# Optimization experiments

Hardware: AMD Instinct MI355X
Metric: run time of the kernel (lower is better)

The kernel has to match this reference:

```python
import jax, jax.numpy as jnp
import numpy as np

N, D, P, R, T, K = 200000, 128, 4096, 4, 3, 16

def setup_inputs() -> dict:
    key = jax.random.key(0)
    ks = jax.random.split(key, 9)
    return {
        "node_embeds": jax.random.normal(ks[0], (N, D), jnp.float32),
        "node_pairs": jax.random.randint(ks[1], (P, 2), 0, N),
        "node_type_ids": jax.random.randint(ks[2], (N,), 0, T),
        "neighbor_idx": jax.random.randint(ks[3], (P, 2, R, K), 0, N),
        "delta_t": jax.random.uniform(ks[4], (P, 2, R, K), jnp.float32),
        "W_phi": jax.random.normal(ks[5], (T, D, D), jnp.float32) * 0.05,
        "W_zeta": jax.random.normal(ks[6], (2 * D,), jnp.float32) * 0.05,
        "W_beta_w": jax.random.normal(ks[7], (R, D, D), jnp.float32) * 0.05,
        "W_beta_b": jax.random.normal(ks[8], (R, D), jnp.float32) * 0.05,
    }

def reference(node_embeds, node_pairs, node_type_ids, neighbor_idx, delta_t,
              W_phi, W_zeta, W_beta_w, W_beta_b):
    n = node_embeds.shape[0]
    # per-node type-specific linear: compute all types then select (T small)
    H_all = jnp.einsum('nd,tde->tne', node_embeds, W_phi)        # [T,N,D]
    H = H_all[node_type_ids, jnp.arange(n)]                      # [N,D]
    # micro attention: e = W_zeta([h_n; h_s]) * exp(-dt), softmax over K neighbors
    zn, zs = W_zeta[:D], W_zeta[D:]
    h_n = H[neighbor_idx]                                        # [P,2,R,K,D]
    e_n = jnp.einsum('psrkd,d->psrk', h_n, zn)
    e_s = jnp.einsum('psd,d->ps', H[node_pairs], zs)             # [P,2]
    e = (e_n + e_s[:, :, None, None]) * jnp.exp(-delta_t)        # [P,2,R,K]
    alpha = jax.nn.softmax(e, axis=-1)
    # meso: attention-weighted aggregation per relation, then per-relation linear
    h_nei = node_embeds[neighbor_idx]                            # [P,2,R,K,D]
    h_agg = jnp.einsum('psrk,psrkd->psrd', alpha, h_nei)         # [P,2,R,D]
    h_beta = jnp.einsum('psrd,rde->psre', h_agg, W_beta_w) + W_beta_b
    # macro: average over both pair sides and relations, sigmoid combine
    x_tilde = h_beta.mean(axis=(1, 2))                           # [P,D]
    return jax.nn.sigmoid(x_tilde)
```

## Files before the change

kernel.cpp:

```cpp
#include <hip/hip_runtime.h>
#include <hip/hip_bf16.h>

#define NN 200000
#define D 128
#define P 4096
#define R 4
#define T 3
#define K 16

__device__ __forceinline__ float bf2f(unsigned int u) {
    union { unsigned int i; float f; } c;
    c.i = u << 16;
    return c.f;
}
__device__ __forceinline__ unsigned short f2bf(float x) {
    union { float f; unsigned int i; } c; c.f = x;
    unsigned int r = c.i + 0x7FFFu + ((c.i >> 16) & 1u);
    return (unsigned short)(r >> 16);
}
__device__ __forceinline__ float ldE(const void* p, size_t i, int f32) {
    return f32 ? ((const float*)p)[i] : bf2f(((const unsigned short*)p)[i]);
}
__device__ __forceinline__ void ld8(const void* p, size_t off, int f32, float* o) {
    if (f32) {
        const float* q = (const float*)p + off;
        float4 a = *(const float4*)q;
        float4 b = *(const float4*)(q + 4);
        o[0]=a.x; o[1]=a.y; o[2]=a.z; o[3]=a.w;
        o[4]=b.x; o[5]=b.y; o[6]=b.z; o[7]=b.w;
    } else {
        uint4 r = *(const uint4*)((const unsigned short*)p + off);
        o[0]=bf2f(r.x & 0xffffu); o[1]=bf2f(r.x >> 16);
        o[2]=bf2f(r.y & 0xffffu); o[3]=bf2f(r.y >> 16);
        o[4]=bf2f(r.z & 0xffffu); o[5]=bf2f(r.z >> 16);
        o[6]=bf2f(r.w & 0xffffu); o[7]=bf2f(r.w >> 16);
    }
}

__global__ void prep_kernel(const unsigned short* __restrict__ emb_u,
                            const void* __restrict__ W_phi,
                            const void* __restrict__ W_zeta,
                            int* __restrict__ gflag,
                            float* __restrict__ ws_v, float* __restrict__ ws_u) {
    __shared__ int sbad[2];
    const int tid = threadIdx.x;
    const int t   = blockIdx.x;
    int bad = 0;
    #pragma unroll
    for (int i = 0; i < 4; ++i) {
        unsigned short u = emb_u[(size_t)(blockIdx.x * 512 + tid * 4 + i) * 2 * 97];
        unsigned int e = (u >> 7) & 0xFFu;
        if (e >= 147u) bad = 1;
    }
    int anyb = __any(bad) ? 1 : 0;
    if ((tid & 63) == 0) sbad[tid >> 6] = anyb;
    __syncthreads();
    const int f32 = sbad[0] | sbad[1];
    if (t == 0 && tid == 0) *gflag = f32;

    const int d = tid;
    const size_t rb = (size_t)(t * D + d) * D;
    float av = 0.f, au = 0.f;
    for (int e = 0; e < D; e += 8) {
        float w[8], zn[8], zs[8];
        ld8(W_phi, rb + e, f32, w);
        ld8(W_zeta, e, f32, zn);
        ld8(W_zeta, D + e, f32, zs);
        #pragma unroll
        for (int q = 0; q < 8; ++q) { av += w[q] * zn[q]; au += w[q] * zs[q]; }
    }
    ws_v[t * D + d] = av;
    ws_u[t * D + d] = au;
}

__global__ __launch_bounds__(256, 8) void fused_all(
    const void* __restrict__ emb,
    const int* __restrict__ pairs,
    const int* __restrict__ types,
    const int* __restrict__ nbr,
    const void* __restrict__ dlt,
    const void* __restrict__ W_bw,
    const void* __restrict__ W_bb,
    const float* __restrict__ ws_v,
    const float* __restrict__ ws_u,
    const int* __restrict__ flag,
    void* __restrict__ out)
{
    __shared__ __align__(16) float vsh[T * D];
    __shared__ __align__(16) float ush[T * D];
    __shared__ __align__(16) float gsh[2][2][R][D];
    __shared__ __align__(16) float ysh[2][2][D];

    const int f32  = *flag;
    const int tid  = threadIdx.x;
    const int wv   = tid >> 6;
    const int l    = tid & 63;
    const int pr   = wv >> 1;
    const int s    = wv & 1;
    const int p    = blockIdx.x * 2 + pr;
    const int rsub = l >> 4;
    const int ch   = l & 15;
    const int base = p * 2 * R * K + s * 64;

    const int nb  = nbr[base + l];
    const float dtv = ldE(dlt, (size_t)base + l, f32);
    const int tp  = types[nb];
    const int ns  = pairs[p * 2 + s];
    const int ts  = types[ns];

    const unsigned short* eu = (const unsigned short*)emb;

    int snb[4];
    #pragma unroll
    for (int i = 0; i < 4; ++i) snb[i] = __shfl(nb, i * 4 + rsub, 64);
    uint4 cur[4] = {};
    float ee0, ee1;
    if (!f32) {
        #pragma unroll
        for (int i = 0; i < 4; ++i)
            cur[i] = *(const uint4*)(eu + (size_t)snb[i] * D + ch * 8);
        unsigned int w2 = *(const unsigned int*)(eu + (size_t)ns * D + 2 * l);
        ee0 = bf2f(w2 & 0xffffu); ee1 = bf2f(w2 >> 16);
    } else {
        float2 f2 = *(const float2*)((const float*)emb + (size_t)ns * D + 2 * l);
        ee0 = f2.x; ee1 = f2.y;
    }

    for (int i = tid; i < T * D; i += 256) { vsh[i] = ws_v[i]; ush[i] = ws_u[i]; }
    __syncthreads();

    float es;
    {
        float a = ee0 * ush[ts * D + 2 * l] + ee1 * ush[ts * D + 2 * l + 1];
        #pragma unroll
        for (int off = 1; off <= 32; off <<= 1) a += __shfl_xor(a, off, 64);
        es = a;
    }

    if (!f32) {
        uint4 nxt[4];
        #pragma unroll
        for (int r = 0; r < R; ++r) {
            float sdt[4]; int stp[4];
            #pragma unroll
            for (int i = 0; i < 4; ++i) {
                int srcl = r * 16 + i * 4 + rsub;
                sdt[i] = __shfl(dtv, srcl, 64);
                stp[i] = __shfl(tp,  srcl, 64);
            }
            if (r < 3) {
                int snb2[4];
                #pragma unroll
                for (int i = 0; i < 4; ++i) snb2[i] = __shfl(nb, (r + 1) * 16 + i * 4 + rsub, 64);
                #pragma unroll
                for (int i = 0; i < 4; ++i)
                    nxt[i] = *(const uint4*)(eu + (size_t)snb2[i] * D + ch * 8);
            }
            float ef[4];
            #pragma unroll
            for (int i = 0; i < 4; ++i) {
                const float* vp = vsh + stp[i] * D + ch * 8;
                float4 v0 = *(const float4*)vp;
                float4 v1 = *(const float4*)(vp + 4);
                float a = 0.f;
                a += bf2f(cur[i].x & 0xffffu) * v0.x + bf2f(cur[i].x >> 16) * v0.y;
                a += bf2f(cur[i].y & 0xffffu) * v0.z + bf2f(cur[i].y >> 16) * v0.w;
                a += bf2f(cur[i].z & 0xffffu) * v1.x + bf2f(cur[i].z >> 16) * v1.y;
                a += bf2f(cur[i].w & 0xffffu) * v1.z + bf2f(cur[i].w >> 16) * v1.w;
                #pragma unroll
                for (int off = 1; off <= 8; off <<= 1) a += __shfl_xor(a, off, 64);
                ef[i] = (a + es) * __expf(-sdt[i]);
            }
            float m = fmaxf(fmaxf(ef[0], ef[1]), fmaxf(ef[2], ef[3]));
            m = fmaxf(m, __shfl_xor(m, 16, 64));
            m = fmaxf(m, __shfl_xor(m, 32, 64));
            float al[4], ssum = 0.f;
            #pragma unroll
            for (int i = 0; i < 4; ++i) { al[i] = __expf(ef[i] - m); ssum += al[i]; }
            ssum += __shfl_xor(ssum, 16, 64);
            ssum += __shfl_xor(ssum, 32, 64);
            float inv = 1.f / ssum;
            float acc[8] = {0.f,0.f,0.f,0.f,0.f,0.f,0.f,0.f};
            #pragma unroll
            for (int i = 0; i < 4; ++i) {
                float a = al[i] * inv;
                acc[0] += a * bf2f(cur[i].x & 0xffffu); acc[1] += a * bf2f(cur[i].x >> 16);
                acc[2] += a * bf2f(cur[i].y & 0xffffu); acc[3] += a * bf2f(cur[i].y >> 16);
                acc[4] += a * bf2f(cur[i].z & 0xffffu); acc[5] += a * bf2f(cur[i].z >> 16);
                acc[6] += a * bf2f(cur[i].w & 0xffffu); acc[7] += a * bf2f(cur[i].w >> 16);
            }
            #pragma unroll
            for (int q = 0; q < 8; ++q) {
                acc[q] += __shfl_xor(acc[q], 16, 64);
                acc[q] += __shfl_xor(acc[q], 32, 64);
            }
            if (rsub == 0) {
                *(float4*)(&gsh[pr][s][r][ch * 8])     = make_float4(acc[0], acc[1], acc[2], acc[3]);
                *(float4*)(&gsh[pr][s][r][ch * 8 + 4]) = make_float4(acc[4], acc[5], acc[6], acc[7]);
            }
            #pragma unroll
            for (int i = 0; i < 4; ++i) cur[i] = nxt[i];
        }
    } else {
        #pragma unroll
        for (int r = 0; r < R; ++r) {
            int snbL[4]; float sdt[4]; int stp[4];
            #pragma unroll
            for (int i = 0; i < 4; ++i) {
                int srcl = r * 16 + i * 4 + rsub;
                snbL[i] = __shfl(nb,  srcl, 64);
                sdt[i] = __shfl(dtv, srcl, 64);
                stp[i] = __shfl(tp,  srcl, 64);
            }
            float ef[4];
            #pragma unroll
            for (int i = 0; i < 4; ++i) {
                const float* vp = vsh + stp[i] * D + ch * 8;
                float rv[8];
                ld8(emb, (size_t)snbL[i] * D + ch * 8, 1, rv);
                float a = 0.f;
                #pragma unroll
                for (int q = 0; q < 8; ++q) a += rv[q] * vp[q];
                #pragma unroll
                for (int off = 1; off <= 8; off <<= 1) a += __shfl_xor(a, off, 64);
                ef[i] = (a + es) * __expf(-sdt[i]);
            }
            float m = fmaxf(fmaxf(ef[0], ef[1]), fmaxf(ef[2], ef[3]));
            m = fmaxf(m, __shfl_xor(m, 16, 64));
            m = fmaxf(m, __shfl_xor(m, 32, 64));
            float al[4], ssum = 0.f;
            #pragma unroll
            for (int i = 0; i < 4; ++i) { al[i] = __expf(ef[i] - m); ssum += al[i]; }
            ssum += __shfl_xor(ssum, 16, 64);
            ssum += __shfl_xor(ssum, 32, 64);
            float inv = 1.f / ssum;
            float acc[8] = {0.f,0.f,0.f,0.f,0.f,0.f,0.f,0.f};
            #pragma unroll
            for (int i = 0; i < 4; ++i) {
                float a = al[i] * inv;
                float rv[8];
                ld8(emb, (size_t)snbL[i] * D + ch * 8, 1, rv);
                #pragma unroll
                for (int q = 0; q < 8; ++q) acc[q] += a * rv[q];
            }
            #pragma unroll
            for (int q = 0; q < 8; ++q) {
                acc[q] += __shfl_xor(acc[q], 16, 64);
                acc[q] += __shfl_xor(acc[q], 32, 64);
            }
            if (rsub == 0) {
                *(float4*)(&gsh[pr][s][r][ch * 8])     = make_float4(acc[0], acc[1], acc[2], acc[3]);
                *(float4*)(&gsh[pr][s][r][ch * 8 + 4]) = make_float4(acc[4], acc[5], acc[6], acc[7]);
            }
        }
    }
    __syncthreads();

    float y[8] = {0.f,0.f,0.f,0.f,0.f,0.f,0.f,0.f};
    const unsigned short* Wu = (const unsigned short*)W_bw;
    #pragma unroll
    for (int rr = 0; rr < 2; ++rr) {
        const int r = s * 2 + rr;
        #pragma unroll 8
        for (int dd = 0; dd < 32; ++dd) {
            const int d = rsub * 32 + ((dd + 8 * rsub) & 31);
            float gd = gsh[pr][0][r][d] + gsh[pr][1][r][d];
            size_t wo = ((size_t)(r * D + d)) * D + ch * 8;
            if (!f32) {
                uint4 wr = *(const uint4*)(Wu + wo);
                y[0] += gd * bf2f(wr.x & 0xffffu); y[1] += gd * bf2f(wr.x >> 16);
                y[2] += gd * bf2f(wr.y & 0xffffu); y[3] += gd * bf2f(wr.y >> 16);
                y[4] += gd * bf2f(wr.z & 0xffffu); y[5] += gd * bf2f(wr.z >> 16);
                y[6] += gd * bf2f(wr.w & 0xffffu); y[7] += gd * bf2f(wr.w >> 16);
            } else {
                float wb[8]; ld8(W_bw, wo, 1, wb);
                #pragma unroll
                for (int q = 0; q < 8; ++q) y[q] += gd * wb[q];
            }
        }
    }
    #pragma unroll
    for (int q = 0; q < 8; ++q) {
        y[q] += __shfl_xor(y[q], 16, 64);
        y[q] += __shfl_xor(y[q], 32, 64);
    }
    if (rsub == 0) {
        *(float4*)(&ysh[pr][s][ch * 8])     = make_float4(y[0], y[1], y[2], y[3]);
        *(float4*)(&ysh[pr][s][ch * 8 + 4]) = make_float4(y[4], y[5], y[6], y[7]);
    }
    __syncthreads();

    if (s == 0 && rsub == 0) {
        float bs[8] = {0.f,0.f,0.f,0.f,0.f,0.f,0.f,0.f};
        #pragma unroll
        for (int r = 0; r < R; ++r) {
            float bb[8]; ld8(W_bb, (size_t)r * D + ch * 8, f32, bb);
            #pragma unroll
            for (int q = 0; q < 8; ++q) bs[q] += bb[q];
        }
        float o[8];
        #pragma unroll
        for (int q = 0; q < 8; ++q) {
            int e = ch * 8 + q;
            float x = (ysh[pr][0][e] + ysh[pr][1][e] + 2.f * bs[q]) * 0.125f;
            o[q] = 1.f / (1.f + __expf(-x));
        }
        size_t ob = (size_t)p * D + ch * 8;
        if (f32) {
            *(float4*)((float*)out + ob)     = make_float4(o[0], o[1], o[2], o[3]);
            *(float4*)((float*)out + ob + 4) = make_float4(o[4], o[5], o[6], o[7]);
        } else {
            uint4 pk;
            pk.x = (unsigned int)f2bf(o[0]) | ((unsigned int)f2bf(o[1]) << 16);
            pk.y = (unsigned int)f2bf(o[2]) | ((unsigned int)f2bf(o[3]) << 16);
            pk.z = (unsigned int)f2bf(o[4]) | ((unsigned int)f2bf(o[5]) << 16);
            pk.w = (unsigned int)f2bf(o[6]) | ((unsigned int)f2bf(o[7]) << 16);
            *(uint4*)((unsigned short*)out + ob) = pk;
        }
    }
}

extern "C" void kernel_launch(void* const* d_in, const int* in_sizes, int n_in,
                              void* d_out, int out_size, void* d_ws, size_t ws_size,
                              hipStream_t stream) {
    const void* emb    = d_in[0];
    const int*  pairs  = (const int*)d_in[1];
    const int*  types  = (const int*)d_in[2];
    const int*  nbr    = (const int*)d_in[3];
    const void* dlt    = d_in[4];
    const void* W_phi  = d_in[5];
    const void* W_zeta = d_in[6];
    const void* W_bw   = d_in[7];
    const void* W_bb   = d_in[8];

    int*   flag = (int*)d_ws;
    float* ws_v = (float*)d_ws + 64;
    float* ws_u = ws_v + T * D;

    prep_kernel<<<dim3(T), dim3(128), 0, stream>>>((const unsigned short*)emb,
                                                   W_phi, W_zeta, flag, ws_v, ws_u);
    fused_all<<<dim3(P / 2), dim3(256), 0, stream>>>(emb, pairs, types, nbr, dlt,
                                                     W_bw, W_bb, ws_v, ws_u, flag, d_out);
}
```

Baseline: 292.5 us.

## Share each W_beta relation slice across both pairs in a block

```diff
diff --git a/kernel.cpp b/kernel.cpp
--- a/kernel.cpp
+++ b/kernel.cpp
@@ -73,7 +73,7 @@
     ws_u[t * D + d] = au;
 }
 
-__global__ __launch_bounds__(256, 8) void fused_all(
+__global__ __launch_bounds__(256, 4) void fused_all(
     const void* __restrict__ emb,
     const int* __restrict__ pairs,
     const int* __restrict__ types,
@@ -89,7 +89,7 @@
     __shared__ __align__(16) float vsh[T * D];
     __shared__ __align__(16) float ush[T * D];
     __shared__ __align__(16) float gsh[2][2][R][D];
-    __shared__ __align__(16) float ysh[2][2][D];
+    __shared__ __align__(16) float ysh[2][R][D];
 
     const int f32  = *flag;
     const int tid  = threadIdx.x;
@@ -256,37 +256,45 @@
     }
     __syncthreads();
 
-    float y[8] = {0.f,0.f,0.f,0.f,0.f,0.f,0.f,0.f};
-    const unsigned short* Wu = (const unsigned short*)W_bw;
-    #pragma unroll
-    for (int rr = 0; rr < 2; ++rr) {
-        const int r = s * 2 + rr;
+    float y0[8] = {0.f,0.f,0.f,0.f,0.f,0.f,0.f,0.f};
+    float y1[8] = {0.f,0.f,0.f,0.f,0.f,0.f,0.f,0.f};
+    {
+        const int rb = wv;
+        const unsigned short* Wu = (const unsigned short*)W_bw;
         #pragma unroll 8
         for (int dd = 0; dd < 32; ++dd) {
             const int d = rsub * 32 + ((dd + 8 * rsub) & 31);
-            float gd = gsh[pr][0][r][d] + gsh[pr][1][r][d];
-            size_t wo = ((size_t)(r * D + d)) * D + ch * 8;
+            const float g0 = gsh[0][0][rb][d] + gsh[0][1][rb][d];
+            const float g1 = gsh[1][0][rb][d] + gsh[1][1][rb][d];
+            const size_t wo = ((size_t)(rb * D + d)) * D + ch * 8;
             if (!f32) {
                 uint4 wr = *(const uint4*)(Wu + wo);
-                y[0] += gd * bf2f(wr.x & 0xffffu); y[1] += gd * bf2f(wr.x >> 16);
-                y[2] += gd * bf2f(wr.y & 0xffffu); y[3] += gd * bf2f(wr.y >> 16);
-                y[4] += gd * bf2f(wr.z & 0xffffu); y[5] += gd * bf2f(wr.z >> 16);
-                y[6] += gd * bf2f(wr.w & 0xffffu); y[7] += gd * bf2f(wr.w >> 16);
+                float w;
+                w = bf2f(wr.x & 0xffffu); y0[0] += g0 * w; y1[0] += g1 * w;
+                w = bf2f(wr.x >> 16);     y0[1] += g0 * w; y1[1] += g1 * w;
+                w = bf2f(wr.y & 0xffffu); y0[2] += g0 * w; y1[2] += g1 * w;
+                w = bf2f(wr.y >> 16);     y0[3] += g0 * w; y1[3] += g1 * w;
+                w = bf2f(wr.z & 0xffffu); y0[4] += g0 * w; y1[4] += g1 * w;
+                w = bf2f(wr.z >> 16);     y0[5] += g0 * w; y1[5] += g1 * w;
+                w = bf2f(wr.w & 0xffffu); y0[6] += g0 * w; y1[6] += g1 * w;
+                w = bf2f(wr.w >> 16);     y0[7] += g0 * w; y1[7] += g1 * w;
             } else {
                 float wb[8]; ld8(W_bw, wo, 1, wb);
                 #pragma unroll
-                for (int q = 0; q < 8; ++q) y[q] += gd * wb[q];
-            }
-        }
-    }
-    #pragma unroll
-    for (int q = 0; q < 8; ++q) {
-        y[q] += __shfl_xor(y[q], 16, 64);
-        y[q] += __shfl_xor(y[q], 32, 64);
-    }
-    if (rsub == 0) {
-        *(float4*)(&ysh[pr][s][ch * 8])     = make_float4(y[0], y[1], y[2], y[3]);
-        *(float4*)(&ysh[pr][s][ch * 8 + 4]) = make_float4(y[4], y[5], y[6], y[7]);
+                for (int q = 0; q < 8; ++q) { y0[q] += g0 * wb[q]; y1[q] += g1 * wb[q]; }
+            }
+        }
+        #pragma unroll
+        for (int q = 0; q < 8; ++q) {
+            y0[q] += __shfl_xor(y0[q], 16, 64); y0[q] += __shfl_xor(y0[q], 32, 64);
+            y1[q] += __shfl_xor(y1[q], 16, 64); y1[q] += __shfl_xor(y1[q], 32, 64);
+        }
+        if (rsub == 0) {
+            *(float4*)(&ysh[0][rb][ch * 8])     = make_float4(y0[0], y0[1], y0[2], y0[3]);
+            *(float4*)(&ysh[0][rb][ch * 8 + 4]) = make_float4(y0[4], y0[5], y0[6], y0[7]);
+            *(float4*)(&ysh[1][rb][ch * 8])     = make_float4(y1[0], y1[1], y1[2], y1[3]);
+            *(float4*)(&ysh[1][rb][ch * 8 + 4]) = make_float4(y1[4], y1[5], y1[6], y1[7]);
+        }
     }
     __syncthreads();
 
@@ -302,7 +310,8 @@
         #pragma unroll
         for (int q = 0; q < 8; ++q) {
             int e = ch * 8 + q;
-            float x = (ysh[pr][0][e] + ysh[pr][1][e] + 2.f * bs[q]) * 0.125f;
+            float x = (ysh[pr][0][e] + ysh[pr][1][e] + ysh[pr][2][e] + ysh[pr][3][e]
+                       + 2.f * bs[q]) * 0.125f;
             o[q] = 1.f / (1.f + __expf(-x));
         }
         size_t ob = (size_t)p * D + ch * 8;
```

New measurement: 251.6 us. 14.0% less time.
